# Kernel optimization log

Measured on AMD Instinct MI355X. Metric: run time of the kernel, lower is better.

The kernel has to match this reference:

```python
import jax, jax.numpy as jnp
import numpy as np

COMMITMENT = 0.25

def setup_inputs() -> dict:
    key = jax.random.key(0)
    k1, k2 = jax.random.split(key)
    x = jax.random.normal(k1, (64, 256, 32, 32), dtype=jnp.float32)
    embed = jax.random.normal(k2, (256, 1024), dtype=jnp.float32)  # [emb_dim, num_emb]
    return {"x": x, "embed": embed}

def reference(x, embed):
    # x: [B, C, H, W] -> NHWC
    xt = jnp.transpose(x, (0, 2, 3, 1))              # [B, H, W, C]
    B, H, W, C = xt.shape
    flat = xt.reshape(-1, C)                         # [N, C]
    # squared euclidean distances to each codebook column
    dist = (jnp.sum(flat * flat, axis=1, keepdims=True)
            - 2.0 * flat @ embed
            + jnp.sum(embed * embed, axis=0, keepdims=True))  # [N, num_emb]
    embed_idx = jnp.argmin(dist, axis=1).reshape(B, H, W)     # [B, H, W]
    quantize = embed.T[embed_idx]                    # [B, H, W, C]
    e_latent_loss = jnp.mean((jax.lax.stop_gradient(quantize) - xt) ** 2)
    q_latent_loss = jnp.mean((quantize - jax.lax.stop_gradient(xt)) ** 2)
    loss = q_latent_loss + COMMITMENT * e_latent_loss
    # straight-through estimator
    quantize = xt + jax.lax.stop_gradient(quantize - xt)
    quantize = jnp.transpose(quantize, (0, 3, 1, 2))  # back to NCHW
    return quantize, loss, embed_idx
```

## Files before the change

### kernel.cpp

```cpp
#include <hip/hip_runtime.h>

#define CDIM 256
#define HW   1024
#define NPIX 65536
#define KDIM 1024
#define TAU  0.5f
#define RB   4

using bf16x8 = __attribute__((ext_vector_type(8))) short;
using f32x4  = __attribute__((ext_vector_type(4))) float;
typedef unsigned int u32;

static __device__ __forceinline__ unsigned short f2bf(float v) {
    union { float f; unsigned u; } a; a.f = v;
    unsigned u = a.u;
    u += 0x7fffu + ((u >> 16) & 1u);
    return (unsigned short)(u >> 16);
}

static __device__ __forceinline__ void gload_lds16(const void* g, void* s) {
    __builtin_amdgcn_global_load_lds(
        (const __attribute__((address_space(1))) u32*)g,
        (__attribute__((address_space(3))) u32*)s,
        16, 0, 0);
}

__global__ void ee_kernel(const float* __restrict__ embed, float* __restrict__ ee) {
    int k = blockIdx.x * 256 + threadIdx.x;
    float s = 0.f;
#pragma unroll 8
    for (int c = 0; c < CDIM; ++c) {
        float v = embed[c * KDIM + k];
        s += v * v;
    }
    ee[k] = s;
}

__global__ void prep_e(const float* __restrict__ embed, short* __restrict__ e_hi) {
    int tid = blockIdx.x * 256 + threadIdx.x;
    int l  = tid & 63;
    int f  = tid >> 6;
    int nf = f & 3;
    int ks = (f >> 2) & 7;
    int nh = (f >> 5) & 1;
    int nt = f >> 6;
    int n  = nt * 128 + (nh * 4 + nf) * 16 + (l & 15);
    int c0 = ks * 32 + (l >> 4) * 8;
    bf16x8 h8;
#pragma unroll
    for (int j = 0; j < 8; ++j)
        h8[j] = (short)f2bf(-2.0f * embed[(c0 + j) * KDIM + n]);
    *(bf16x8*)&e_hi[(size_t)tid * 8] = h8;
}

__launch_bounds__(256, 1)
__global__ void vq_gemm(const float* __restrict__ x, const short* __restrict__ e_hi,
                        const float* __restrict__ ee, int* __restrict__ idx_out,
                        int* __restrict__ worklist, int* __restrict__ wcount) {
    __shared__ short Bs[2][16384];
    const int t  = threadIdx.x;
    const int l  = t & 63;
    const int w  = t >> 6;
    const int lr = l & 15;
    const int lg = l >> 4;
    const int px0 = blockIdx.x * 256 + w * 64;
    const int b   = px0 >> 10;
    const int p0  = px0 & 1023;
    const float* xb = x + (size_t)b * CDIM * HW;

    bf16x8 a[4][8];
#pragma unroll
    for (int mf = 0; mf < 4; ++mf) {
#pragma unroll
        for (int ks = 0; ks < 8; ++ks) {
            const float* p = xb + (size_t)(ks * 32 + lg * 8) * HW + p0 + mf * 16 + lr;
            float v[8];
#pragma unroll
            for (int j = 0; j < 8; ++j) v[j] = p[(size_t)j * HW];
#pragma unroll
            for (int j = 0; j < 8; ++j) a[mf][ks][j] = (short)f2bf(v[j]);
        }
    }

    float minv[16], min2v[16];
    int   mini[16];
#pragma unroll
    for (int r = 0; r < 16; ++r) { minv[r] = 3.4e38f; min2v[r] = 3.4e38f; mini[r] = 0; }

    {
        const char* src = (const char*)e_hi + w * 8192 + l * 16;
        char* dst = (char*)&Bs[0][0] + w * 8192;
#pragma unroll
        for (int i = 0; i < 8; ++i)
            gload_lds16(src + i * 1024, dst + i * 1024);
    }
    __syncthreads();

    for (int ch = 0; ch < 16; ++ch) {
        const int cur = ch & 1;
        if (ch < 15) {
            const char* src = (const char*)e_hi + (size_t)(ch + 1) * 32768 + w * 8192 + l * 16;
            char* dst = (char*)&Bs[cur ^ 1][0] + w * 8192;
#pragma unroll
            for (int i = 0; i < 8; ++i)
                gload_lds16(src + i * 1024, dst + i * 1024);
        }

        f32x4 acc[4][4];
#pragma unroll
        for (int mf = 0; mf < 4; ++mf)
#pragma unroll
            for (int nf = 0; nf < 4; ++nf)
                acc[mf][nf] = (f32x4){0.f, 0.f, 0.f, 0.f};

#pragma unroll
        for (int ks = 0; ks < 8; ++ks) {
#pragma unroll
            for (int nf = 0; nf < 4; ++nf) {
                bf16x8 bh = *(const bf16x8*)&Bs[cur][((ks * 4 + nf) * 64 + l) * 8];
#pragma unroll
                for (int mf = 0; mf < 4; ++mf)
                    acc[mf][nf] = __builtin_amdgcn_mfma_f32_16x16x32_bf16(a[mf][ks], bh, acc[mf][nf], 0, 0, 0);
            }
        }

#pragma unroll
        for (int nf = 0; nf < 4; ++nf) {
            const int kg = ch * 64 + nf * 16 + lr;
            const float eev = ee[kg];
#pragma unroll
            for (int mf = 0; mf < 4; ++mf)
#pragma unroll
                for (int j = 0; j < 4; ++j) {
                    const int r = mf * 4 + j;
                    float m = acc[mf][nf][j] + eev;
                    bool lt = m < minv[r];
                    float sec = lt ? minv[r] : m;
                    minv[r] = lt ? m : minv[r];
                    mini[r] = lt ? kg : mini[r];
                    min2v[r] = fminf(min2v[r], sec);
                }
        }
        __syncthreads();
    }

#pragma unroll
    for (int r = 0; r < 16; ++r) {
        float v1 = minv[r]; int i1 = mini[r]; float v2 = min2v[r];
#pragma unroll
        for (int mask = 1; mask < 16; mask <<= 1) {
            float ov1 = __shfl_xor(v1, mask, 64);
            int   oi1 = __shfl_xor(i1, mask, 64);
            float ov2 = __shfl_xor(v2, mask, 64);
            float vmax = fmaxf(v1, ov1);
            v2 = fminf(fminf(v2, ov2), vmax);
            bool take = (ov1 < v1) || (ov1 == v1 && oi1 < i1);
            v1 = take ? ov1 : v1;
            i1 = take ? oi1 : i1;
        }
        if (lr == 0) {
            int px = px0 + (r >> 2) * 16 + lg * 4 + (r & 3);
            idx_out[px] = i1;
            if (v2 - v1 < TAU) {
                int pos = atomicAdd(wcount, 1);
                worklist[pos] = px;
            }
        }
    }
}

__launch_bounds__(256)
__global__ void vq_rescue(const float* __restrict__ x, const float* __restrict__ embed,
                          const float* __restrict__ ee,
                          const int* __restrict__ worklist, const int* __restrict__ wcount,
                          int* __restrict__ idx_out) {
    __shared__ float xs[RB][CDIM];
    __shared__ int   pxs[RB];
    __shared__ float redv[4][RB];
    __shared__ int   redi[4][RB];
    const int t  = threadIdx.x;
    const int wv = t >> 6, ln = t & 63;
    const int cnt = *wcount;
    for (int base = blockIdx.x * RB; base < cnt; base += gridDim.x * RB) {
        const int nb = min(RB, cnt - base);
        __syncthreads();
        if (t < RB) pxs[t] = worklist[base + (t < nb ? t : nb - 1)];
        __syncthreads();
#pragma unroll
        for (int i = 0; i < RB; ++i) {
            int gn = pxs[i];
            xs[i][t] = x[(size_t)(gn >> 10) * CDIM * HW + (size_t)t * HW + (gn & 1023)];
        }
        __syncthreads();

        float4 acc[RB];
#pragma unroll
        for (int i = 0; i < RB; ++i) acc[i] = make_float4(0.f, 0.f, 0.f, 0.f);
#pragma unroll 4
        for (int c = 0; c < CDIM; ++c) {
            float4 ev = *(const float4*)&embed[c * KDIM + t * 4];
#pragma unroll
            for (int i = 0; i < RB; ++i) {
                float xv = xs[i][c];
                acc[i].x = fmaf(xv, ev.x, acc[i].x);
                acc[i].y = fmaf(xv, ev.y, acc[i].y);
                acc[i].z = fmaf(xv, ev.z, acc[i].z);
                acc[i].w = fmaf(xv, ev.w, acc[i].w);
            }
        }
        const float4 eev = *(const float4*)&ee[t * 4];
#pragma unroll
        for (int i = 0; i < RB; ++i) {
            float d0 = fmaf(-2.f, acc[i].x, eev.x);
            float d1 = fmaf(-2.f, acc[i].y, eev.y);
            float d2 = fmaf(-2.f, acc[i].z, eev.z);
            float d3 = fmaf(-2.f, acc[i].w, eev.w);
            float v = d0; int ix = t * 4;
            if (d1 < v) { v = d1; ix = t * 4 + 1; }
            if (d2 < v) { v = d2; ix = t * 4 + 2; }
            if (d3 < v) { v = d3; ix = t * 4 + 3; }
#pragma unroll
            for (int mask = 1; mask < 64; mask <<= 1) {
                float ov = __shfl_xor(v, mask, 64);
                int   oi = __shfl_xor(ix, mask, 64);
                bool take = (ov < v) || (ov == v && oi < ix);
                v = take ? ov : v; ix = take ? oi : ix;
            }
            if (ln == 0) { redv[wv][i] = v; redi[wv][i] = ix; }
        }
        __syncthreads();
        if (t < nb) {
            float fv = redv[0][t]; int fi = redi[0][t];
#pragma unroll
            for (int q = 1; q < 4; ++q) {
                float v = redv[q][t]; int ix = redi[q][t];
                if (v < fv || (v == fv && ix < fi)) { fv = v; fi = ix; }
            }
            idx_out[pxs[t]] = fi;
        }
    }
}

__launch_bounds__(256)
__global__ void vq_epilogue(const float* __restrict__ x, const float* __restrict__ embed,
                            const int* __restrict__ idx_in, float* __restrict__ out_q,
                            float* __restrict__ out_idx, float* __restrict__ partials) {
    __shared__ int idxs[128];
    __shared__ float lred[4];
    const int t = threadIdx.x;
    const int n0 = blockIdx.x * 128;
    const int b = n0 >> 10;
    const int pix0 = n0 & 1023;
    const size_t xbase = (size_t)b * CDIM * HW + pix0;

    if (t < 128) {
        int iv = idx_in[n0 + t];
        idxs[t] = iv;
        out_idx[n0 + t] = (float)iv;
    }
    __syncthreads();

    const int pp = (t & 63) * 2;
    const int c0 = t >> 6;
    const int i0 = idxs[pp], i1 = idxs[pp + 1];
    float lsum = 0.f;
    for (int c = c0; c < CDIM; c += 4) {
        float2 xv = *(const float2*)&x[xbase + (size_t)c * HW + pp];
        float q0 = embed[c * KDIM + i0];
        float q1 = embed[c * KDIM + i1];
        *(float2*)&out_q[xbase + (size_t)c * HW + pp] = make_float2(q0, q1);
        float d0 = q0 - xv.x, d1 = q1 - xv.y;
        lsum = fmaf(d0, d0, lsum);
        lsum = fmaf(d1, d1, lsum);
    }
#pragma unroll
    for (int off = 32; off > 0; off >>= 1)
        lsum += __shfl_down(lsum, off, 64);
    if ((t & 63) == 0) lred[t >> 6] = lsum;
    __syncthreads();
    if (t == 0)
        partials[blockIdx.x] = (lred[0] + lred[1]) + (lred[2] + lred[3]);
}

__global__ void loss_kernel(const float* __restrict__ partials, float* __restrict__ out_loss) {
    __shared__ float s[256];
    s[threadIdx.x] = partials[threadIdx.x] + partials[threadIdx.x + 256];
    __syncthreads();
    for (int off = 128; off > 0; off >>= 1) {
        if (threadIdx.x < off) s[threadIdx.x] += s[threadIdx.x + off];
        __syncthreads();
    }
    if (threadIdx.x == 0)
        out_loss[0] = 1.25f * s[0] / 16777216.0f;
}

extern "C" void kernel_launch(void* const* d_in, const int* in_sizes, int n_in,
                              void* d_out, int out_size, void* d_ws, size_t ws_size,
                              hipStream_t stream) {
    const float* x     = (const float*)d_in[0];
    const float* embed = (const float*)d_in[1];
    float* out_q    = (float*)d_out;
    float* out_loss = out_q + (size_t)NPIX * CDIM;
    float* out_idx  = out_loss + 1;
    int*   idx_i32  = (int*)out_idx;

    short* e_hi     = (short*)out_q;
    int*   worklist = (int*)(out_q + 131072);

    float* ws       = (float*)d_ws;
    float* ee       = ws;
    int*   wcount   = (int*)(ws + 1024);
    float* partials = ws + 1024 + 64;

    ee_kernel<<<KDIM / 256, 256, 0, stream>>>(embed, ee);
    prep_e<<<128, 256, 0, stream>>>(embed, e_hi);
    hipMemsetAsync(wcount, 0, 4, stream);
    vq_gemm<<<NPIX / 256, 256, 0, stream>>>(x, e_hi, ee, idx_i32, worklist, wcount);
    vq_rescue<<<1024, 256, 0, stream>>>(x, embed, ee, worklist, wcount, idx_i32);
    vq_epilogue<<<NPIX / 128, 256, 0, stream>>>(x, embed, idx_i32, out_q, out_idx, partials);
    loss_kernel<<<1, 256, 0, stream>>>(partials, out_loss);
}
```

Before: 186.6 us.

## Split codebook across two GEMM blocks and stage gathered codes in LDS

The GEMM grid doubles to 512 blocks. Each block scans half the codebook and writes its per-pixel best, second-best and index to scratch, and a new merge kernel combines the two halves and builds the rescue worklist. The epilogue now gathers codebook rows from a transposed copy of embed, made by a new transpose kernel when the workspace is big enough, into a swizzled LDS tile, so both the gather reads and the NCHW writes are coalesced. This is meant to raise occupancy on the GEMM and fix the scattered embed gathers, at the cost of the extra kernel launches and scratch traffic.

After: 194.2 us. 4.1% more time.

```diff
diff --git a/kernel.cpp b/kernel.cpp
--- a/kernel.cpp
+++ b/kernel.cpp
@@ -6,6 +6,7 @@
 #define KDIM 1024
 #define TAU  0.5f
 #define RB   4
+#define SWZ(c) (((c) & 31) ^ (((c) >> 3) & 24))
 
 using bf16x8 = __attribute__((ext_vector_type(8))) short;
 using f32x4  = __attribute__((ext_vector_type(4))) float;
@@ -34,6 +35,25 @@
         s += v * v;
     }
     ee[k] = s;
+}
+
+__global__ void transpose_e(const float* __restrict__ embed, float* __restrict__ embedT) {
+    __shared__ float tl[32][33];
+    const int t = threadIdx.x;
+    const int j = t & 31, r = t >> 5;
+    const int k0 = (blockIdx.x & 31) * 32;
+    const int c0 = (blockIdx.x >> 5) * 32;
+#pragma unroll
+    for (int rr = 0; rr < 4; ++rr) {
+        int c = r * 4 + rr;
+        tl[c][j] = embed[(size_t)(c0 + c) * KDIM + k0 + j];
+    }
+    __syncthreads();
+#pragma unroll
+    for (int rr = 0; rr < 4; ++rr) {
+        int k = r * 4 + rr;
+        embedT[(size_t)(k0 + k) * CDIM + c0 + j] = tl[j][k];
+    }
 }
 
 __global__ void prep_e(const float* __restrict__ embed, short* __restrict__ e_hi) {
@@ -53,21 +73,33 @@
     *(bf16x8*)&e_hi[(size_t)tid * 8] = h8;
 }
 
-__launch_bounds__(256, 1)
+__launch_bounds__(256)
 __global__ void vq_gemm(const float* __restrict__ x, const short* __restrict__ e_hi,
-                        const float* __restrict__ ee, int* __restrict__ idx_out,
-                        int* __restrict__ worklist, int* __restrict__ wcount) {
+                        const float* __restrict__ ee,
+                        float* __restrict__ hv1, float* __restrict__ hv2,
+                        int* __restrict__ hidx) {
     __shared__ short Bs[2][16384];
     const int t  = threadIdx.x;
     const int l  = t & 63;
     const int w  = t >> 6;
     const int lr = l & 15;
     const int lg = l >> 4;
-    const int px0 = blockIdx.x * 256 + w * 64;
+    const int tile = blockIdx.x & 255;
+    const int half = blockIdx.x >> 8;
+    const int ch0  = half * 8;
+    const int px0 = tile * 256 + w * 64;
     const int b   = px0 >> 10;
     const int p0  = px0 & 1023;
     const float* xb = x + (size_t)b * CDIM * HW;
 
+    {
+        const char* src = (const char*)e_hi + (size_t)ch0 * 32768 + w * 8192 + l * 16;
+        char* dst = (char*)&Bs[0][0] + w * 8192;
+#pragma unroll
+        for (int i = 0; i < 8; ++i)
+            gload_lds16(src + i * 1024, dst + i * 1024);
+    }
+
     bf16x8 a[4][8];
 #pragma unroll
     for (int mf = 0; mf < 4; ++mf) {
@@ -87,19 +119,12 @@
 #pragma unroll
     for (int r = 0; r < 16; ++r) { minv[r] = 3.4e38f; min2v[r] = 3.4e38f; mini[r] = 0; }
 
-    {
-        const char* src = (const char*)e_hi + w * 8192 + l * 16;
-        char* dst = (char*)&Bs[0][0] + w * 8192;
-#pragma unroll
-        for (int i = 0; i < 8; ++i)
-            gload_lds16(src + i * 1024, dst + i * 1024);
-    }
-    __syncthreads();
-
-    for (int ch = 0; ch < 16; ++ch) {
-        const int cur = ch & 1;
-        if (ch < 15) {
-            const char* src = (const char*)e_hi + (size_t)(ch + 1) * 32768 + w * 8192 + l * 16;
+    __syncthreads();
+
+    for (int cc = 0; cc < 8; ++cc) {
+        const int cur = cc & 1;
+        if (cc < 7) {
+            const char* src = (const char*)e_hi + (size_t)(ch0 + cc + 1) * 32768 + w * 8192 + l * 16;
             char* dst = (char*)&Bs[cur ^ 1][0] + w * 8192;
 #pragma unroll
             for (int i = 0; i < 8; ++i)
@@ -126,7 +151,7 @@
 
 #pragma unroll
         for (int nf = 0; nf < 4; ++nf) {
-            const int kg = ch * 64 + nf * 16 + lr;
+            const int kg = (ch0 + cc) * 64 + nf * 16 + lr;
             const float eev = ee[kg];
 #pragma unroll
             for (int mf = 0; mf < 4; ++mf)
@@ -160,12 +185,27 @@
         }
         if (lr == 0) {
             int px = px0 + (r >> 2) * 16 + lg * 4 + (r & 3);
-            idx_out[px] = i1;
-            if (v2 - v1 < TAU) {
-                int pos = atomicAdd(wcount, 1);
-                worklist[pos] = px;
-            }
-        }
+            int o = half * NPIX + px;
+            hv1[o] = v1; hv2[o] = v2; hidx[o] = i1;
+        }
+    }
+}
+
+__global__ void merge_halves(const float* __restrict__ hv1, const float* __restrict__ hv2,
+                             const int* __restrict__ hidx, int* __restrict__ idx_out,
+                             int* __restrict__ worklist, int* __restrict__ wcount) {
+    int px = blockIdx.x * 256 + threadIdx.x;
+    float va = hv1[px],        vb = hv1[NPIX + px];
+    float sa = hv2[px],        sb = hv2[NPIX + px];
+    int   ia = hidx[px],       ib = hidx[NPIX + px];
+    bool aw = va <= vb;
+    float v1 = aw ? va : vb;
+    int   i1 = aw ? ia : ib;
+    float v2 = fminf(aw ? sa : sb, aw ? vb : va);
+    idx_out[px] = i1;
+    if (v2 - v1 < TAU) {
+        int pos = atomicAdd(wcount, 1);
+        worklist[pos] = px;
     }
 }
 
@@ -243,40 +283,66 @@
 
 __launch_bounds__(256)
 __global__ void vq_epilogue(const float* __restrict__ x, const float* __restrict__ embed,
+                            const float* __restrict__ embedT, int useT,
                             const int* __restrict__ idx_in, float* __restrict__ out_q,
                             float* __restrict__ out_idx, float* __restrict__ partials) {
-    __shared__ int idxs[128];
+    __shared__ float q[16384];
+    __shared__ int   idxs[128];
     __shared__ float lred[4];
     const int t = threadIdx.x;
+    const int w = t >> 6, l = t & 63;
     const int n0 = blockIdx.x * 128;
-    const int b = n0 >> 10;
-    const int pix0 = n0 & 1023;
-    const size_t xbase = (size_t)b * CDIM * HW + pix0;
-
-    if (t < 128) {
-        int iv = idx_in[n0 + t];
-        idxs[t] = iv;
-        out_idx[n0 + t] = (float)iv;
-    }
-    __syncthreads();
-
-    const int pp = (t & 63) * 2;
-    const int c0 = t >> 6;
-    const int i0 = idxs[pp], i1 = idxs[pp + 1];
+    const int b  = n0 >> 10;
+
+    if (t < 128) idxs[t] = idx_in[n0 + t];
+    __syncthreads();
+    if (t < 128) out_idx[n0 + t] = (float)idxs[t];
+
+    const int j  = t >> 2;
+    const int qd = t & 3;
     float lsum = 0.f;
-    for (int c = c0; c < CDIM; c += 4) {
-        float2 xv = *(const float2*)&x[xbase + (size_t)c * HW + pp];
-        float q0 = embed[c * KDIM + i0];
-        float q1 = embed[c * KDIM + i1];
-        *(float2*)&out_q[xbase + (size_t)c * HW + pp] = make_float2(q0, q1);
-        float d0 = q0 - xv.x, d1 = q1 - xv.y;
-        lsum = fmaf(d0, d0, lsum);
-        lsum = fmaf(d1, d1, lsum);
-    }
+
+#pragma unroll
+    for (int pass = 0; pass < 2; ++pass) {
+        const int myidx = idxs[pass * 64 + j];
+        if (useT) {
+            const float4* src4 = (const float4*)embedT + (size_t)myidx * 64;
+#pragma unroll
+            for (int i = 0; i < 16; ++i) {
+                float4 v = src4[qd * 16 + i];
+                int c = qd * 64 + i * 4;
+                q[(c + 0) * 64 + (j ^ SWZ(c + 0))] = v.x;
+                q[(c + 1) * 64 + (j ^ SWZ(c + 1))] = v.y;
+                q[(c + 2) * 64 + (j ^ SWZ(c + 2))] = v.z;
+                q[(c + 3) * 64 + (j ^ SWZ(c + 3))] = v.w;
+            }
+        } else {
+#pragma unroll 4
+            for (int i = 0; i < 64; ++i) {
+                int c = qd * 64 + i;
+                q[c * 64 + (j ^ SWZ(c))] = embed[(size_t)c * KDIM + myidx];
+            }
+        }
+        __syncthreads();
+
+        const int p0 = (n0 & 1023) + pass * 64;
+        const size_t xbase = (size_t)b * CDIM * HW + p0;
+#pragma unroll 8
+        for (int ci = 0; ci < 64; ++ci) {
+            int c = w * 64 + ci;
+            float qv = q[c * 64 + (l ^ SWZ(c))];
+            float xv = x[xbase + (size_t)c * HW + l];
+            out_q[xbase + (size_t)c * HW + l] = qv;
+            float d = qv - xv;
+            lsum = fmaf(d, d, lsum);
+        }
+        __syncthreads();
+    }
+
 #pragma unroll
     for (int off = 32; off > 0; off >>= 1)
         lsum += __shfl_down(lsum, off, 64);
-    if ((t & 63) == 0) lred[t >> 6] = lsum;
+    if (l == 0) lred[w] = lsum;
     __syncthreads();
     if (t == 0)
         partials[blockIdx.x] = (lred[0] + lred[1]) + (lred[2] + lred[3]);
@@ -306,17 +372,25 @@
 
     short* e_hi     = (short*)out_q;
     int*   worklist = (int*)(out_q + 131072);
+    float* hv1      = out_q + 196608;
+    float* hv2      = out_q + 327680;
+    int*   hidx     = (int*)(out_q + 458752);
 
     float* ws       = (float*)d_ws;
     float* ee       = ws;
     int*   wcount   = (int*)(ws + 1024);
-    float* partials = ws + 1024 + 64;
+    float* partials = ws + 1088;
+    float* embedT   = ws + 1600;
+    int useT = (ws_size >= (size_t)(1600 + 262144) * sizeof(float)) ? 1 : 0;
 
     ee_kernel<<<KDIM / 256, 256, 0, stream>>>(embed, ee);
+    if (useT) transpose_e<<<256, 256, 0, stream>>>(embed, embedT);
     prep_e<<<128, 256, 0, stream>>>(embed, e_hi);
     hipMemsetAsync(wcount, 0, 4, stream);
-    vq_gemm<<<NPIX / 256, 256, 0, stream>>>(x, e_hi, ee, idx_i32, worklist, wcount);
+    vq_gemm<<<512, 256, 0, stream>>>(x, e_hi, ee, hv1, hv2, hidx);
+    merge_halves<<<NPIX / 256, 256, 0, stream>>>(hv1, hv2, hidx, idx_i32, worklist, wcount);
     vq_rescue<<<1024, 256, 0, stream>>>(x, embed, ee, worklist, wcount, idx_i32);
-    vq_epilogue<<<NPIX / 128, 256, 0, stream>>>(x, embed, idx_i32, out_q, out_idx, partials);
+    vq_epilogue<<<NPIX / 128, 256, 0, stream>>>(x, embed, useT ? embedT : embed, useT,
+                                                idx_i32, out_q, out_idx, partials);
     loss_kernel<<<1, 256, 0, stream>>>(partials, out_loss);
 }
```
